# Optimization experiments

Hardware: AMD Instinct MI355X
Metric: run time of the kernel (lower is better)

## Reference

```python
import jax, jax.numpy as jnp
import numpy as np

N, E = 8000, 128000
IN_DIM = OUT_DIM = REL_DIM = 64
NUM_RELS, NUM_BASES = 200, 50
R2 = 2 * NUM_RELS


def setup_inputs() -> dict:
    key = jax.random.key(0)
    ks = jax.random.split(key, 10)
    feat = jax.random.normal(ks[0], (N, IN_DIM), jnp.float32)
    rel_emb = jax.random.normal(ks[1], (R2, REL_DIM), jnp.float32)
    weight = jax.random.normal(ks[2], (NUM_BASES, IN_DIM, OUT_DIM), jnp.float32) * 0.05
    w_comp = jax.random.normal(ks[3], (R2, NUM_BASES), jnp.float32) * 0.1
    self_loop_weight = jax.random.normal(ks[4], (IN_DIM, OUT_DIM), jnp.float32) * 0.05
    W_R_w = jax.random.normal(ks[5], (REL_DIM, REL_DIM), jnp.float32) * 0.05
    W_R_b = jnp.zeros((REL_DIM,), jnp.float32)
    src = jax.random.randint(ks[6], (E,), 0, N, dtype=jnp.int32)
    dst = jax.random.randint(ks[7], (E,), 0, N, dtype=jnp.int32)
    etype = jax.random.randint(ks[8], (E,), 0, R2, dtype=jnp.int32)
    return dict(feat=feat, rel_emb=rel_emb, weight=weight, w_comp=w_comp,
                self_loop_weight=self_loop_weight, W_R_w=W_R_w, W_R_b=W_R_b,
                src=src, dst=dst, etype=etype)


def reference(feat, rel_emb, weight, w_comp, self_loop_weight, W_R_w, W_R_b,
              src, dst, etype):
    # rel_weight = (w_comp @ weight.view(B, in*out)).view(R2, in, out)
    rel_weight = jnp.einsum('rb,bio->rio', w_comp, weight)          # [R2, in, out]
    # msg_func: per-edge relation weight gather + bmm (gather-mm pattern)
    w_e = rel_weight[etype]                                          # [E, in, out]
    msg = jnp.einsum('ei,eio->eo', feat[src], w_e)                   # [E, out]
    # aggregator: alpha = 1/in_deg(dst) per edge -> weighted sum == mean over mailbox
    ones = jnp.ones((msg.shape[0],), msg.dtype)
    in_deg = jax.ops.segment_sum(ones, dst, num_segments=N)          # [N]
    nei_sum = jax.ops.segment_sum(msg, dst, num_segments=N)          # [N, out]
    nei_msg = nei_sum / jnp.maximum(in_deg, 1.0)[:, None]
    # curr_emb = dst_feat @ self_loop_weight (same for every edge into a node)
    curr_emb = feat @ self_loop_weight                               # [N, out]
    h = curr_emb + nei_msg                                           # no bias / no activation
    # is_input_layer=True: repr = cat([feat, h])
    repr_ = jnp.concatenate([feat, h], axis=1)                       # [N, in+out]
    # edge_update: W_R linear on relation embeddings (act is None)
    rel_emb_new = rel_emb @ W_R_w.T + W_R_b                          # [R2, rel_dim]
    return repr_, rel_emb_new
```

## Files before the change

kernel.cpp:

```cpp
#include <hip/hip_runtime.h>

#define N_NODES 8000
#define E_EDGES 128000
#define NUM_BASES 50
#define R2 400
#define CPR 4
#define RT 16

static __device__ __forceinline__ float bf2f(unsigned short u) {
    return __uint_as_float(((unsigned int)u) << 16);
}
static __device__ __forceinline__ unsigned short f2bf(float f) {
    unsigned int u = __float_as_uint(f);
    u += 0x7fffu + ((u >> 16) & 1u);
    return (unsigned short)(u >> 16);
}
static __device__ __forceinline__ float bcast(float v, int lane) {
    return __uint_as_float(__builtin_amdgcn_readlane(__float_as_uint(v), lane));
}

__global__ __launch_bounds__(256) void k_pre(const float* __restrict__ w_comp,
                                             const float* __restrict__ weight,
                                             unsigned short* __restrict__ relWh,
                                             const int* __restrict__ dst,
                                             const int* __restrict__ etype,
                                             int* __restrict__ cnt16,
                                             int* __restrict__ dcnt) {
    const int blk = blockIdx.x;
    const int t = threadIdx.x;
    if (blk < 100) {
        const int rt = blk >> 2;
        const int pb = blk & 3;
        const int r0 = rt * RT;
        const int p = pb * 256 + t;
        const float4* w4 = (const float4*)weight;
        float4 acc[RT];
#pragma unroll
        for (int rr = 0; rr < RT; ++rr) acc[rr] = make_float4(0.f, 0.f, 0.f, 0.f);
        for (int b = 0; b < NUM_BASES; ++b) {
            const float4 w = w4[b * 1024 + p];
#pragma unroll
            for (int rr = 0; rr < RT; ++rr) {
                const float c = w_comp[(r0 + rr) * NUM_BASES + b];
                acc[rr].x = fmaf(c, w.x, acc[rr].x);
                acc[rr].y = fmaf(c, w.y, acc[rr].y);
                acc[rr].z = fmaf(c, w.z, acc[rr].z);
                acc[rr].w = fmaf(c, w.w, acc[rr].w);
            }
        }
        ushort4* outh = (ushort4*)relWh;
#pragma unroll
        for (int rr = 0; rr < RT; ++rr) {
            ushort4 v;
            v.x = f2bf(acc[rr].x); v.y = f2bf(acc[rr].y);
            v.z = f2bf(acc[rr].z); v.w = f2bf(acc[rr].w);
            outh[(r0 + rr) * 1024 + p] = v;
        }
    } else {
        const int e = (blk - 100) * 256 + t;
        if (e >= E_EDGES) return;
        atomicAdd(&cnt16[etype[e] * 16], 1);
        atomicAdd(&dcnt[dst[e]], 1);
    }
}

__global__ __launch_bounds__(1024) void k_scan(const int* __restrict__ cnt16,
                                               const int* __restrict__ dcnt,
                                               int* __restrict__ off,
                                               int* __restrict__ doff) {
    __shared__ int s[1024];
    const int t = threadIdx.x;
    if (blockIdx.x == 0) {
        s[t] = (t < R2) ? cnt16[t * 16] : 0;
        __syncthreads();
        for (int d = 1; d < 1024; d <<= 1) {
            const int v = (t >= d) ? s[t - d] : 0;
            __syncthreads();
            s[t] += v;
            __syncthreads();
        }
        if (t == 0) off[0] = 0;
        if (t < R2) off[t + 1] = s[t];
    } else {
        const int base = t * 8;
        int loc[8];
        int run = 0;
#pragma unroll
        for (int q = 0; q < 8; ++q) {
            const int v = (base + q < N_NODES) ? dcnt[base + q] : 0;
            loc[q] = run;
            run += v;
        }
        s[t] = run;
        __syncthreads();
        for (int d = 1; d < 1024; d <<= 1) {
            const int v = (t >= d) ? s[t - d] : 0;
            __syncthreads();
            s[t] += v;
            __syncthreads();
        }
        const int ex = s[t] - run;
#pragma unroll
        for (int q = 0; q < 8; ++q)
            if (base + q < N_NODES) doff[base + q] = ex + loc[q];
        if (t == 1023) doff[N_NODES] = s[1023];
    }
}

__global__ __launch_bounds__(256) void k_scatter(const int* __restrict__ src,
                                                 const int* __restrict__ dst,
                                                 const int* __restrict__ etype,
                                                 const int* __restrict__ off,
                                                 const int* __restrict__ doff,
                                                 int* __restrict__ cursor16,
                                                 int* __restrict__ dcursor,
                                                 int* __restrict__ ssrc,
                                                 int* __restrict__ sdst,
                                                 int* __restrict__ dperm) {
    const int e = blockIdx.x * 256 + threadIdx.x;
    if (e >= E_EDGES) return;
    const int r = etype[e];
    const int rpos = off[r] + atomicAdd(&cursor16[r * 16], 1);
    ssrc[rpos] = src[e];
    sdst[rpos] = dst[e];
    const int d = dst[e];
    const int dpos = doff[d] + atomicAdd(&dcursor[d], 1);
    dperm[dpos] = rpos;
}

__global__ __launch_bounds__(256) void k_edge(const float* __restrict__ feat,
                                              const unsigned short* __restrict__ relWh,
                                              const int* __restrict__ ssrc,
                                              const int* __restrict__ off,
                                              unsigned short* __restrict__ msg) {
    const int xcd = blockIdx.x & 7;
    const int j = blockIdx.x >> 3;
    const int r = xcd * 50 + (j >> 2);
    const int chunk = j & 3;
    const int lane = threadIdx.x & 63;
    const int wv = threadIdx.x >> 6;
    const int beg = off[r];
    const int cnt = off[r + 1] - beg;
    const int cbeg = beg + (cnt * chunk) / CPR;
    const int cend = beg + (cnt * (chunk + 1)) / CPR;

    const unsigned short* __restrict__ Wh = relWh + r * 4096;
    float w[64];
#pragma unroll
    for (int i = 0; i < 64; ++i) w[i] = bf2f(Wh[i * 64 + lane]);

    int idx = cbeg + wv;
    for (; idx + 4 < cend; idx += 8) {
        const int iB = idx + 4;
        const int sA = __builtin_amdgcn_readfirstlane(ssrc[idx]);
        const int sB = __builtin_amdgcn_readfirstlane(ssrc[iB]);
        const float* __restrict__ fA = feat + sA * 64;
        const float* __restrict__ fB = feat + sB * 64;
        float a0 = 0.f, a1 = 0.f, a2 = 0.f, a3 = 0.f;
        float b0 = 0.f, b1 = 0.f, b2 = 0.f, b3 = 0.f;
#pragma unroll
        for (int i = 0; i < 64; i += 4) {
            a0 = fmaf(fA[i    ], w[i    ], a0);  b0 = fmaf(fB[i    ], w[i    ], b0);
            a1 = fmaf(fA[i + 1], w[i + 1], a1);  b1 = fmaf(fB[i + 1], w[i + 1], b1);
            a2 = fmaf(fA[i + 2], w[i + 2], a2);  b2 = fmaf(fB[i + 2], w[i + 2], b2);
            a3 = fmaf(fA[i + 3], w[i + 3], a3);  b3 = fmaf(fB[i + 3], w[i + 3], b3);
        }
        msg[idx * 64 + lane] = f2bf((a0 + a1) + (a2 + a3));
        msg[iB * 64 + lane] = f2bf((b0 + b1) + (b2 + b3));
    }
    for (; idx < cend; idx += 4) {
        const int s = __builtin_amdgcn_readfirstlane(ssrc[idx]);
        const float* __restrict__ frow = feat + s * 64;
        float a0 = 0.f, a1 = 0.f, a2 = 0.f, a3 = 0.f;
#pragma unroll
        for (int i = 0; i < 64; i += 4) {
            a0 = fmaf(frow[i    ], w[i    ], a0);
            a1 = fmaf(frow[i + 1], w[i + 1], a1);
            a2 = fmaf(frow[i + 2], w[i + 2], a2);
            a3 = fmaf(frow[i + 3], w[i + 3], a3);
        }
        msg[idx * 64 + lane] = f2bf((a0 + a1) + (a2 + a3));
    }
}

__global__ __launch_bounds__(256) void k_edge_at(const float* __restrict__ feat,
                                                 const unsigned short* __restrict__ relWh,
                                                 const int* __restrict__ ssrc,
                                                 const int* __restrict__ sdst,
                                                 const int* __restrict__ off,
                                                 float* __restrict__ nei_sum) {
    const int xcd = blockIdx.x & 7;
    const int j = blockIdx.x >> 3;
    const int r = xcd * 50 + (j >> 2);
    const int chunk = j & 3;
    const int lane = threadIdx.x & 63;
    const int wv = threadIdx.x >> 6;
    const int beg = off[r];
    const int cnt = off[r + 1] - beg;
    const int cbeg = beg + (cnt * chunk) / CPR;
    const int cend = beg + (cnt * (chunk + 1)) / CPR;

    const unsigned short* __restrict__ Wh = relWh + r * 4096;
    float w[64];
#pragma unroll
    for (int i = 0; i < 64; ++i) w[i] = bf2f(Wh[i * 64 + lane]);

    for (int idx = cbeg + wv; idx < cend; idx += 4) {
        const int s = __builtin_amdgcn_readfirstlane(ssrc[idx]);
        const int d = __builtin_amdgcn_readfirstlane(sdst[idx]);
        const float* __restrict__ frow = feat + s * 64;
        float a0 = 0.f, a1 = 0.f, a2 = 0.f, a3 = 0.f;
#pragma unroll
        for (int i = 0; i < 64; i += 4) {
            a0 = fmaf(frow[i    ], w[i    ], a0);
            a1 = fmaf(frow[i + 1], w[i + 1], a1);
            a2 = fmaf(frow[i + 2], w[i + 2], a2);
            a3 = fmaf(frow[i + 3], w[i + 3], a3);
        }
        atomicAdd(&nei_sum[d * 64 + lane], (a0 + a1) + (a2 + a3));
    }
}

__global__ __launch_bounds__(256) void k_post(const float* __restrict__ feat,
                                              const float* __restrict__ slw,
                                              const int* __restrict__ doff,
                                              const int* __restrict__ dperm,
                                              const unsigned short* __restrict__ msg,
                                              const float* __restrict__ rel_emb,
                                              const float* __restrict__ Wr,
                                              const float* __restrict__ br,
                                              float* __restrict__ out) {
    __shared__ float s_w[4096];
    const int blk = blockIdx.x;
    const int t = threadIdx.x;
    const int lane = t & 63;
    const int wv = t >> 6;
    if (blk < 500) {
#pragma unroll
        for (int k = 0; k < 16; ++k) s_w[k * 256 + t] = slw[k * 256 + t];
        __syncthreads();
#pragma unroll
        for (int q = 0; q < 4; ++q) {
            const int n = blk * 16 + wv * 4 + q;
            const int b0 = doff[n];
            const int b1 = doff[n + 1];
            const float* __restrict__ frow = feat + n * 64;
            const float fa = frow[lane];
            float acc = 0.f;
#pragma unroll
            for (int i = 0; i < 64; ++i)
                acc = fmaf(frow[i], s_w[i * 64 + lane], acc);
            float sm = 0.f;
            int jj = b0;
            for (; jj + 1 < b1; jj += 2) {
                const int r0 = dperm[jj];
                const int r1 = dperm[jj + 1];
                sm += bf2f(msg[r0 * 64 + lane]) + bf2f(msg[r1 * 64 + lane]);
            }
            if (jj < b1) sm += bf2f(msg[dperm[jj] * 64 + lane]);
            const float inv = 1.0f / fmaxf((float)(b1 - b0), 1.0f);
            out[n * 128 + lane] = fa;
            out[n * 128 + 64 + lane] = fmaf(sm, inv, acc);
        }
    } else {
#pragma unroll
        for (int k = 0; k < 16; ++k) {
            const int idx = k * 256 + t;
            s_w[(idx & 63) * 64 + (idx >> 6)] = Wr[idx];
        }
        __syncthreads();
        const int r = (blk - 500) * 4 + wv;
        const float re = rel_emb[r * 64 + lane];
        float acc = br[lane];
#pragma unroll
        for (int k = 0; k < 64; ++k)
            acc = fmaf(bcast(re, k), s_w[k * 64 + lane], acc);
        out[N_NODES * 128 + r * 64 + lane] = acc;
    }
}

__global__ __launch_bounds__(256) void k_post_at(const float* __restrict__ feat,
                                                 const float* __restrict__ slw,
                                                 const float* __restrict__ nei_sum,
                                                 const int* __restrict__ dcnt,
                                                 const float* __restrict__ rel_emb,
                                                 const float* __restrict__ Wr,
                                                 const float* __restrict__ br,
                                                 float* __restrict__ out) {
    __shared__ float s_w[4096];
    const int blk = blockIdx.x;
    const int t = threadIdx.x;
    const int lane = t & 63;
    const int wv = t >> 6;
    if (blk < 500) {
#pragma unroll
        for (int k = 0; k < 16; ++k) s_w[k * 256 + t] = slw[k * 256 + t];
        __syncthreads();
#pragma unroll
        for (int q = 0; q < 4; ++q) {
            const int n = blk * 16 + wv * 4 + q;
            const float* __restrict__ frow = feat + n * 64;
            const float fa = frow[lane];
            float acc = 0.f;
#pragma unroll
            for (int i = 0; i < 64; ++i)
                acc = fmaf(frow[i], s_w[i * 64 + lane], acc);
            const float inv = 1.0f / fmaxf((float)dcnt[n], 1.0f);
            out[n * 128 + lane] = fa;
            out[n * 128 + 64 + lane] = fmaf(nei_sum[n * 64 + lane], inv, acc);
        }
    } else {
#pragma unroll
        for (int k = 0; k < 16; ++k) {
            const int idx = k * 256 + t;
            s_w[(idx & 63) * 64 + (idx >> 6)] = Wr[idx];
        }
        __syncthreads();
        const int r = (blk - 500) * 4 + wv;
        const float re = rel_emb[r * 64 + lane];
        float acc = br[lane];
#pragma unroll
        for (int k = 0; k < 64; ++k)
            acc = fmaf(bcast(re, k), s_w[k * 64 + lane], acc);
        out[N_NODES * 128 + r * 64 + lane] = acc;
    }
}

extern "C" void kernel_launch(void* const* d_in, const int* in_sizes, int n_in,
                              void* d_out, int out_size, void* d_ws, size_t ws_size,
                              hipStream_t stream) {
    const float* feat    = (const float*)d_in[0];
    const float* rel_emb = (const float*)d_in[1];
    const float* weight  = (const float*)d_in[2];
    const float* w_comp  = (const float*)d_in[3];
    const float* slw     = (const float*)d_in[4];
    const float* Wr      = (const float*)d_in[5];
    const float* br      = (const float*)d_in[6];
    const int*   src     = (const int*)d_in[7];
    const int*   dst     = (const int*)d_in[8];
    const int*   etype   = (const int*)d_in[9];
    float* out = (float*)d_out;
    char* ws = (char*)d_ws;

    if (ws_size >= 21345728) {
        unsigned short* relWh = (unsigned short*)(ws);
        unsigned short* msg   = (unsigned short*)(ws + 3276800);
        int* ssrc     = (int*)(ws + 19660800);
        int* sdst     = (int*)(ws + 20172800);
        int* dperm    = (int*)(ws + 20684800);
        int* off      = (int*)(ws + 21196800);
        int* doff     = (int*)(ws + 21198464);
        int* cnt16    = (int*)(ws + 21230528);
        int* cursor16 = (int*)(ws + 21256128);
        int* dcnt     = (int*)(ws + 21281728);
        int* dcursor  = (int*)(ws + 21313728);

        hipMemsetAsync(cnt16, 0, 115200, stream);
        k_pre<<<600, 256, 0, stream>>>(w_comp, weight, relWh, dst, etype,
                                       cnt16, dcnt);
        k_scan<<<2, 1024, 0, stream>>>(cnt16, dcnt, off, doff);
        k_scatter<<<500, 256, 0, stream>>>(src, dst, etype, off, doff,
                                           cursor16, dcursor, ssrc, sdst, dperm);
        k_edge<<<R2 * CPR, 256, 0, stream>>>(feat, relWh, ssrc, off, msg);
        k_post<<<600, 256, 0, stream>>>(feat, slw, doff, dperm, msg,
                                        rel_emb, Wr, br, out);
    } else {
        unsigned short* relWh = (unsigned short*)(ws);
        int* ssrc     = (int*)(ws + 3276800);
        int* sdst     = (int*)(ws + 3788800);
        int* dperm    = (int*)(ws + 4300800);
        int* off      = (int*)(ws + 4812800);
        int* doff     = (int*)(ws + 4814464);
        float* nei    = (float*)(ws + 4846528);
        int* cnt16    = (int*)(ws + 6894528);
        int* cursor16 = (int*)(ws + 6920128);
        int* dcnt     = (int*)(ws + 6945728);
        int* dcursor  = (int*)(ws + 6977728);

        hipMemsetAsync(nei, 0, 2163200, stream);
        k_pre<<<600, 256, 0, stream>>>(w_comp, weight, relWh, dst, etype,
                                       cnt16, dcnt);
        k_scan<<<2, 1024, 0, stream>>>(cnt16, dcnt, off, doff);
        k_scatter<<<500, 256, 0, stream>>>(src, dst, etype, off, doff,
                                           cursor16, dcursor, ssrc, sdst, dperm);
        k_edge_at<<<R2 * CPR, 256, 0, stream>>>(feat, relWh, ssrc, sdst, off, nei);
        k_post_at<<<600, 256, 0, stream>>>(feat, slw, nei, dcnt,
                                           rel_emb, Wr, br, out);
    }
}
```

Baseline: 124.7 us.

## Scatter messages directly to dst-sorted slots and pack edge indices as int2

The scan kernel now seeds the relation and destination cursors with the exclusive offsets, so the scatter kernel gets absolute positions straight from its atomics. Each relation-sorted edge now stores a packed (src, dst-slot) pair. The edge kernel writes each message directly into its destination-sorted slot, which removes the dperm indirection from the aggregation kernel and makes its reads contiguous. The costs are scattered bf16 message writes in the edge kernel and an int2 load per edge. The memset also shrinks, since the cursors no longer need zeroing.

New measurement: 119.5 us. 1.04x faster.

```diff
diff --git a/kernel.cpp b/kernel.cpp
--- a/kernel.cpp
+++ b/kernel.cpp
@@ -67,20 +67,26 @@
 __global__ __launch_bounds__(1024) void k_scan(const int* __restrict__ cnt16,
                                                const int* __restrict__ dcnt,
                                                int* __restrict__ off,
-                                               int* __restrict__ doff) {
+                                               int* __restrict__ doff,
+                                               int* __restrict__ cursor16,
+                                               int* __restrict__ dcursor) {
     __shared__ int s[1024];
     const int t = threadIdx.x;
     if (blockIdx.x == 0) {
-        s[t] = (t < R2) ? cnt16[t * 16] : 0;
+        const int v = (t < R2) ? cnt16[t * 16] : 0;
+        s[t] = v;
         __syncthreads();
         for (int d = 1; d < 1024; d <<= 1) {
-            const int v = (t >= d) ? s[t - d] : 0;
+            const int p = (t >= d) ? s[t - d] : 0;
             __syncthreads();
-            s[t] += v;
+            s[t] += p;
             __syncthreads();
         }
         if (t == 0) off[0] = 0;
-        if (t < R2) off[t + 1] = s[t];
+        if (t < R2) {
+            off[t + 1] = s[t];
+            cursor16[t * 16] = s[t] - v;
+        }
     } else {
         const int base = t * 8;
         int loc[8];
@@ -94,15 +100,20 @@
         s[t] = run;
         __syncthreads();
         for (int d = 1; d < 1024; d <<= 1) {
-            const int v = (t >= d) ? s[t - d] : 0;
+            const int p = (t >= d) ? s[t - d] : 0;
             __syncthreads();
-            s[t] += v;
+            s[t] += p;
             __syncthreads();
         }
         const int ex = s[t] - run;
 #pragma unroll
-        for (int q = 0; q < 8; ++q)
-            if (base + q < N_NODES) doff[base + q] = ex + loc[q];
+        for (int q = 0; q < 8; ++q) {
+            if (base + q < N_NODES) {
+                const int o = ex + loc[q];
+                doff[base + q] = o;
+                dcursor[base + q] = o;
+            }
+        }
         if (t == 1023) doff[N_NODES] = s[1023];
     }
 }
@@ -110,27 +121,24 @@
 __global__ __launch_bounds__(256) void k_scatter(const int* __restrict__ src,
                                                  const int* __restrict__ dst,
                                                  const int* __restrict__ etype,
-                                                 const int* __restrict__ off,
-                                                 const int* __restrict__ doff,
                                                  int* __restrict__ cursor16,
                                                  int* __restrict__ dcursor,
-                                                 int* __restrict__ ssrc,
-                                                 int* __restrict__ sdst,
-                                                 int* __restrict__ dperm) {
+                                                 int2* __restrict__ sedge,
+                                                 int mode) {
     const int e = blockIdx.x * 256 + threadIdx.x;
     if (e >= E_EDGES) return;
     const int r = etype[e];
-    const int rpos = off[r] + atomicAdd(&cursor16[r * 16], 1);
-    ssrc[rpos] = src[e];
-    sdst[rpos] = dst[e];
     const int d = dst[e];
-    const int dpos = doff[d] + atomicAdd(&dcursor[d], 1);
-    dperm[dpos] = rpos;
+    const int rpos = atomicAdd(&cursor16[r * 16], 1);
+    int y;
+    if (mode == 0) y = atomicAdd(&dcursor[d], 1);
+    else           y = d;
+    sedge[rpos] = make_int2(src[e], y);
 }
 
 __global__ __launch_bounds__(256) void k_edge(const float* __restrict__ feat,
                                               const unsigned short* __restrict__ relWh,
-                                              const int* __restrict__ ssrc,
+                                              const int2* __restrict__ sedge,
                                               const int* __restrict__ off,
                                               unsigned short* __restrict__ msg) {
     const int xcd = blockIdx.x & 7;
@@ -152,8 +160,12 @@
     int idx = cbeg + wv;
     for (; idx + 4 < cend; idx += 8) {
         const int iB = idx + 4;
-        const int sA = __builtin_amdgcn_readfirstlane(ssrc[idx]);
-        const int sB = __builtin_amdgcn_readfirstlane(ssrc[iB]);
+        const int2 eA = sedge[idx];
+        const int2 eB = sedge[iB];
+        const int sA = __builtin_amdgcn_readfirstlane(eA.x);
+        const int dA = __builtin_amdgcn_readfirstlane(eA.y);
+        const int sB = __builtin_amdgcn_readfirstlane(eB.x);
+        const int dB = __builtin_amdgcn_readfirstlane(eB.y);
         const float* __restrict__ fA = feat + sA * 64;
         const float* __restrict__ fB = feat + sB * 64;
         float a0 = 0.f, a1 = 0.f, a2 = 0.f, a3 = 0.f;
@@ -165,12 +177,14 @@
             a2 = fmaf(fA[i + 2], w[i + 2], a2);  b2 = fmaf(fB[i + 2], w[i + 2], b2);
             a3 = fmaf(fA[i + 3], w[i + 3], a3);  b3 = fmaf(fB[i + 3], w[i + 3], b3);
         }
-        msg[idx * 64 + lane] = f2bf((a0 + a1) + (a2 + a3));
-        msg[iB * 64 + lane] = f2bf((b0 + b1) + (b2 + b3));
+        msg[dA * 64 + lane] = f2bf((a0 + a1) + (a2 + a3));
+        msg[dB * 64 + lane] = f2bf((b0 + b1) + (b2 + b3));
     }
     for (; idx < cend; idx += 4) {
-        const int s = __builtin_amdgcn_readfirstlane(ssrc[idx]);
-        const float* __restrict__ frow = feat + s * 64;
+        const int2 eA = sedge[idx];
+        const int sA = __builtin_amdgcn_readfirstlane(eA.x);
+        const int dA = __builtin_amdgcn_readfirstlane(eA.y);
+        const float* __restrict__ frow = feat + sA * 64;
         float a0 = 0.f, a1 = 0.f, a2 = 0.f, a3 = 0.f;
 #pragma unroll
         for (int i = 0; i < 64; i += 4) {
@@ -179,14 +193,13 @@
             a2 = fmaf(frow[i + 2], w[i + 2], a2);
             a3 = fmaf(frow[i + 3], w[i + 3], a3);
         }
-        msg[idx * 64 + lane] = f2bf((a0 + a1) + (a2 + a3));
+        msg[dA * 64 + lane] = f2bf((a0 + a1) + (a2 + a3));
     }
 }
 
 __global__ __launch_bounds__(256) void k_edge_at(const float* __restrict__ feat,
                                                  const unsigned short* __restrict__ relWh,
-                                                 const int* __restrict__ ssrc,
-                                                 const int* __restrict__ sdst,
+                                                 const int2* __restrict__ sedge,
                                                  const int* __restrict__ off,
                                                  float* __restrict__ nei_sum) {
     const int xcd = blockIdx.x & 7;
@@ -206,8 +219,9 @@
     for (int i = 0; i < 64; ++i) w[i] = bf2f(Wh[i * 64 + lane]);
 
     for (int idx = cbeg + wv; idx < cend; idx += 4) {
-        const int s = __builtin_amdgcn_readfirstlane(ssrc[idx]);
-        const int d = __builtin_amdgcn_readfirstlane(sdst[idx]);
+        const int2 eA = sedge[idx];
+        const int s = __builtin_amdgcn_readfirstlane(eA.x);
+        const int d = __builtin_amdgcn_readfirstlane(eA.y);
         const float* __restrict__ frow = feat + s * 64;
         float a0 = 0.f, a1 = 0.f, a2 = 0.f, a3 = 0.f;
 #pragma unroll
@@ -224,7 +238,6 @@
 __global__ __launch_bounds__(256) void k_post(const float* __restrict__ feat,
                                               const float* __restrict__ slw,
                                               const int* __restrict__ doff,
-                                              const int* __restrict__ dperm,
                                               const unsigned short* __restrict__ msg,
                                               const float* __restrict__ rel_emb,
                                               const float* __restrict__ Wr,
@@ -253,11 +266,11 @@
             float sm = 0.f;
             int jj = b0;
             for (; jj + 1 < b1; jj += 2) {
-                const int r0 = dperm[jj];
-                const int r1 = dperm[jj + 1];
-                sm += bf2f(msg[r0 * 64 + lane]) + bf2f(msg[r1 * 64 + lane]);
+                const float m0 = bf2f(msg[jj * 64 + lane]);
+                const float m1 = bf2f(msg[(jj + 1) * 64 + lane]);
+                sm += m0 + m1;
             }
-            if (jj < b1) sm += bf2f(msg[dperm[jj] * 64 + lane]);
+            if (jj < b1) sm += bf2f(msg[jj * 64 + lane]);
             const float inv = 1.0f / fmaxf((float)(b1 - b0), 1.0f);
             out[n * 128 + lane] = fa;
             out[n * 128 + 64 + lane] = fmaf(sm, inv, acc);
@@ -282,7 +295,7 @@
 __global__ __launch_bounds__(256) void k_post_at(const float* __restrict__ feat,
                                                  const float* __restrict__ slw,
                                                  const float* __restrict__ nei_sum,
-                                                 const int* __restrict__ dcnt,
+                                                 const int* __restrict__ doff,
                                                  const float* __restrict__ rel_emb,
                                                  const float* __restrict__ Wr,
                                                  const float* __restrict__ br,
@@ -305,7 +318,8 @@
 #pragma unroll
             for (int i = 0; i < 64; ++i)
                 acc = fmaf(frow[i], s_w[i * 64 + lane], acc);
-            const float inv = 1.0f / fmaxf((float)dcnt[n], 1.0f);
+            const float deg = (float)(doff[n + 1] - doff[n]);
+            const float inv = 1.0f / fmaxf(deg, 1.0f);
             out[n * 128 + lane] = fa;
             out[n * 128 + 64 + lane] = fmaf(nei_sum[n * 64 + lane], inv, acc);
         }
@@ -342,49 +356,45 @@
     float* out = (float*)d_out;
     char* ws = (char*)d_ws;
 
-    if (ws_size >= 21345728) {
+    if (ws_size >= 20833728) {
         unsigned short* relWh = (unsigned short*)(ws);
         unsigned short* msg   = (unsigned short*)(ws + 3276800);
-        int* ssrc     = (int*)(ws + 19660800);
-        int* sdst     = (int*)(ws + 20172800);
-        int* dperm    = (int*)(ws + 20684800);
-        int* off      = (int*)(ws + 21196800);
-        int* doff     = (int*)(ws + 21198464);
-        int* cnt16    = (int*)(ws + 21230528);
-        int* cursor16 = (int*)(ws + 21256128);
-        int* dcnt     = (int*)(ws + 21281728);
-        int* dcursor  = (int*)(ws + 21313728);
-
-        hipMemsetAsync(cnt16, 0, 115200, stream);
+        int2* sedge   = (int2*)(ws + 19660800);
+        int* off      = (int*)(ws + 20684800);
+        int* doff     = (int*)(ws + 20686464);
+        int* cnt16    = (int*)(ws + 20718528);
+        int* dcnt     = (int*)(ws + 20744128);
+        int* cursor16 = (int*)(ws + 20776128);
+        int* dcursor  = (int*)(ws + 20801728);
+
+        hipMemsetAsync(cnt16, 0, 57600, stream);
         k_pre<<<600, 256, 0, stream>>>(w_comp, weight, relWh, dst, etype,
                                        cnt16, dcnt);
-        k_scan<<<2, 1024, 0, stream>>>(cnt16, dcnt, off, doff);
-        k_scatter<<<500, 256, 0, stream>>>(src, dst, etype, off, doff,
-                                           cursor16, dcursor, ssrc, sdst, dperm);
-        k_edge<<<R2 * CPR, 256, 0, stream>>>(feat, relWh, ssrc, off, msg);
-        k_post<<<600, 256, 0, stream>>>(feat, slw, doff, dperm, msg,
-                                        rel_emb, Wr, br, out);
+        k_scan<<<2, 1024, 0, stream>>>(cnt16, dcnt, off, doff, cursor16, dcursor);
+        k_scatter<<<500, 256, 0, stream>>>(src, dst, etype, cursor16, dcursor,
+                                           sedge, 0);
+        k_edge<<<R2 * CPR, 256, 0, stream>>>(feat, relWh, sedge, off, msg);
+        k_post<<<600, 256, 0, stream>>>(feat, slw, doff, msg, rel_emb, Wr, br,
+                                        out);
     } else {
         unsigned short* relWh = (unsigned short*)(ws);
-        int* ssrc     = (int*)(ws + 3276800);
-        int* sdst     = (int*)(ws + 3788800);
-        int* dperm    = (int*)(ws + 4300800);
-        int* off      = (int*)(ws + 4812800);
-        int* doff     = (int*)(ws + 4814464);
-        float* nei    = (float*)(ws + 4846528);
-        int* cnt16    = (int*)(ws + 6894528);
-        int* cursor16 = (int*)(ws + 6920128);
-        int* dcnt     = (int*)(ws + 6945728);
-        int* dcursor  = (int*)(ws + 6977728);
-
-        hipMemsetAsync(nei, 0, 2163200, stream);
+        int2* sedge   = (int2*)(ws + 3276800);
+        int* off      = (int*)(ws + 4300800);
+        int* doff     = (int*)(ws + 4302464);
+        float* nei    = (float*)(ws + 4334528);
+        int* cnt16    = (int*)(ws + 6382528);
+        int* dcnt     = (int*)(ws + 6408128);
+        int* cursor16 = (int*)(ws + 6440128);
+        int* dcursor  = (int*)(ws + 6465728);
+
+        hipMemsetAsync(nei, 0, 2105600, stream);
         k_pre<<<600, 256, 0, stream>>>(w_comp, weight, relWh, dst, etype,
                                        cnt16, dcnt);
-        k_scan<<<2, 1024, 0, stream>>>(cnt16, dcnt, off, doff);
-        k_scatter<<<500, 256, 0, stream>>>(src, dst, etype, off, doff,
-                                           cursor16, dcursor, ssrc, sdst, dperm);
-        k_edge_at<<<R2 * CPR, 256, 0, stream>>>(feat, relWh, ssrc, sdst, off, nei);
-        k_post_at<<<600, 256, 0, stream>>>(feat, slw, nei, dcnt,
-                                           rel_emb, Wr, br, out);
-    }
-}
+        k_scan<<<2, 1024, 0, stream>>>(cnt16, dcnt, off, doff, cursor16, dcursor);
+        k_scatter<<<500, 256, 0, stream>>>(src, dst, etype, cursor16, dcursor,
+                                           sedge, 1);
+        k_edge_at<<<R2 * CPR, 256, 0, stream>>>(feat, relWh, sedge, off, nei);
+        k_post_at<<<600, 256, 0, stream>>>(feat, slw, nei, doff, rel_emb, Wr, br,
+                                           out);
+    }
+}
```
